# Kernel optimization log

Hardware: AMD Instinct MI355X
Metric: run time of the kernel (lower is better)

Reference implementation:

```python
import jax, jax.numpy as jnp
import numpy as np

DIAG_FLOOR = 0.1
DIAG_CEIL = 1.0


def setup_inputs() -> dict:
    key = jax.random.key(0)
    k1, k2, k3, k4 = jax.random.split(key, 4)
    m, in_f, out_f = 16384, 1024, 2048
    z = jax.random.normal(k1, (m, in_f), dtype=jnp.float32)
    diag_params = jax.random.normal(k2, (out_f, in_f), dtype=jnp.float32)
    mean_params = 5.0 * jax.random.normal(k3, (out_f, in_f, 1), dtype=jnp.float32)
    scale_params = jax.random.normal(k4, (out_f,), dtype=jnp.float32)
    return {"z": z, "diag_params": diag_params, "mean_params": mean_params,
            "scale_params": scale_params}


def reference(z, diag_params, mean_params, scale_params):
    # Clamp diag to (0.1, 1.0) via sigmoid; clamp scale via tanh.
    d = DIAG_FLOOR + (DIAG_CEIL - DIAG_FLOOR) * jax.nn.sigmoid(diag_params)  # (out, in)
    mean = mean_params[..., 0]  # (out, in)

    # Diagonal covariance => quadratic forms reduce to elementwise products:
    # z_cov_z[m,k]    = sum_i d[k,i] * z[m,i]^2
    # mean_cov_mean[k]= sum_i d[k,i] * mean[k,i]^2
    # z_cov_mean[m,k] = sum_i z[m,i] * d[k,i] * mean[k,i]
    z_cov_z = jnp.einsum('mi,ki->mk', z * z, d)          # (m, out)
    mean_cov_mean = jnp.sum(d * mean * mean, axis=1)      # (out,)
    z_cov_mean = jnp.einsum('mi,ki->mk', z, d * mean)     # (m, out)

    scaling = jnp.tanh(scale_params)                      # (out,)
    return scaling * jnp.exp(-z_cov_z - mean_cov_mean + 2.0 * z_cov_mean)
```

## Files before the change

### kernel.cpp

```cpp
#include <hip/hip_runtime.h>
#include <hip/hip_bf16.h>
#include <cstdint>
#include <cstddef>

#define M_DIM 16384
#define IN_F  1024
#define OUT_F 2048
#define K_CAT 2048

typedef float f32x4 __attribute__((ext_vector_type(4)));
typedef short short8 __attribute__((ext_vector_type(8)));

__device__ __forceinline__ void gld_lds16(const void* gptr, void* lptr) {
    __builtin_amdgcn_global_load_lds(
        (const __attribute__((address_space(1))) uint32_t*)gptr,
        (__attribute__((address_space(3))) uint32_t*)lptr,
        16 , 0 , 0 );
}

__global__ __launch_bounds__(256) void prep_z_kernel(const float* __restrict__ z,
                                                     __hip_bfloat16* __restrict__ A) {
    const int idx = blockIdx.x * 256 + threadIdx.x;
    const float4 v = ((const float4*)z)[idx];
    const int m  = idx >> 8;
    const int c4 = (idx & 255) * 4;
    __hip_bfloat16 q[4], r[4];
    q[0] = __float2bfloat16(v.x * v.x); r[0] = __float2bfloat16(v.x);
    q[1] = __float2bfloat16(v.y * v.y); r[1] = __float2bfloat16(v.y);
    q[2] = __float2bfloat16(v.z * v.z); r[2] = __float2bfloat16(v.z);
    q[3] = __float2bfloat16(v.w * v.w); r[3] = __float2bfloat16(v.w);
    __hip_bfloat16* rowp = A + (size_t)m * K_CAT;
    *(uint2*)&rowp[c4]        = *(uint2*)q;
    *(uint2*)&rowp[IN_F + c4] = *(uint2*)r;
}

__global__ __launch_bounds__(256) void prep_b_kernel(const float* __restrict__ diag,
                                                     const float* __restrict__ mean,
                                                     const float* __restrict__ scale,
                                                     __hip_bfloat16* __restrict__ B,
                                                     float* __restrict__ mcm,
                                                     float* __restrict__ ts) {
    const int k = blockIdx.x;
    const int t = threadIdx.x;
    const float4 dp = ((const float4*)(diag + (size_t)k * IN_F))[t];
    const float4 mp = ((const float4*)(mean + (size_t)k * IN_F))[t];
    const float dx[4] = {dp.x, dp.y, dp.z, dp.w};
    const float mx[4] = {mp.x, mp.y, mp.z, mp.w};
    __hip_bfloat16 nb[4], pb[4];
    float acc = 0.f;
#pragma unroll
    for (int j = 0; j < 4; ++j) {
        const float d = 0.1f + 0.9f / (1.f + __expf(-dx[j]));
        nb[j] = __float2bfloat16(-d);
        pb[j] = __float2bfloat16(2.f * d * mx[j]);
        acc += d * mx[j] * mx[j];
    }
    __hip_bfloat16* rowp = B + (size_t)k * K_CAT;
    *(uint2*)&rowp[t * 4]        = *(uint2*)nb;
    *(uint2*)&rowp[IN_F + t * 4] = *(uint2*)pb;
#pragma unroll
    for (int off = 32; off > 0; off >>= 1) acc += __shfl_down(acc, off);
    __shared__ float red[4];
    if ((t & 63) == 0) red[t >> 6] = acc;
    __syncthreads();
    if (t == 0) {
        mcm[k] = red[0] + red[1] + red[2] + red[3];
        ts[k]  = tanhf(scale[k]);
    }
}

__global__ __launch_bounds__(256) void gemm_exp_kernel(
    const __hip_bfloat16* __restrict__ A,
    const __hip_bfloat16* __restrict__ B,
    const float* __restrict__ mcm,
    const float* __restrict__ ts,
    float* __restrict__ out) {
    __shared__ __align__(16) __hip_bfloat16 As[128][64];
    __shared__ __align__(16) __hip_bfloat16 Bs[128][64];

    const int t  = threadIdx.x;
    const int bx = blockIdx.x;
    const int tn = bx & 15;
    const int tm = bx >> 4;

    const int lrow  = t >> 3;
    const int lcol8 = (t & 7) * 8;
    const int wid  = t >> 6;
    const int lane = t & 63;
    const int wm = (wid >> 1) * 64;
    const int wn = (wid & 1) * 64;
    const int l15 = lane & 15;
    const int l4  = lane >> 4;

    f32x4 acc[4][4] = {};

    const __hip_bfloat16* aptr = A + (size_t)(tm * 128 + lrow) * K_CAT + lcol8;
    const __hip_bfloat16* bptr = B + (size_t)(tn * 128 + lrow) * K_CAT + lcol8;

    for (int kt = 0; kt < K_CAT / 64; ++kt) {
#pragma unroll
        for (int j = 0; j < 4; ++j) {
            gld_lds16(aptr + (size_t)j * 32 * K_CAT, &As[j * 32 + lrow][lcol8]);
            gld_lds16(bptr + (size_t)j * 32 * K_CAT, &Bs[j * 32 + lrow][lcol8]);
        }
        aptr += 64;
        bptr += 64;
        __syncthreads();

        short8 af[4][2], bfr[4][2];
#pragma unroll
        for (int fm = 0; fm < 4; ++fm)
#pragma unroll
            for (int kk = 0; kk < 2; ++kk)
                af[fm][kk] = *(const short8*)&As[wm + fm * 16 + l15][kk * 32 + l4 * 8];
#pragma unroll
        for (int fn = 0; fn < 4; ++fn)
#pragma unroll
            for (int kk = 0; kk < 2; ++kk)
                bfr[fn][kk] = *(const short8*)&Bs[wn + fn * 16 + l15][kk * 32 + l4 * 8];
#pragma unroll
        for (int kk = 0; kk < 2; ++kk)
#pragma unroll
            for (int fm = 0; fm < 4; ++fm)
#pragma unroll
                for (int fn = 0; fn < 4; ++fn)
                    acc[fm][fn] = __builtin_amdgcn_mfma_f32_16x16x32_bf16(
                        af[fm][kk], bfr[fn][kk], acc[fm][fn], 0, 0, 0);
        __syncthreads();
    }

#pragma unroll
    for (int fn = 0; fn < 4; ++fn) {
        const int ng = tn * 128 + wn + fn * 16 + l15;
        const float tsv = ts[ng];
        const float mv  = mcm[ng];
#pragma unroll
        for (int fm = 0; fm < 4; ++fm) {
            const int mg0 = tm * 128 + wm + fm * 16 + l4 * 4;
#pragma unroll
            for (int r = 0; r < 4; ++r) {
                out[(size_t)(mg0 + r) * OUT_F + ng] = tsv * __expf(acc[fm][fn][r] - mv);
            }
        }
    }
}

extern "C" void kernel_launch(void* const* d_in, const int* in_sizes, int n_in,
                              void* d_out, int out_size, void* d_ws, size_t ws_size,
                              hipStream_t stream) {
    const float* z     = (const float*)d_in[0];
    const float* diag  = (const float*)d_in[1];
    const float* mean  = (const float*)d_in[2];
    const float* scale = (const float*)d_in[3];
    float* out = (float*)d_out;

    char* ws = (char*)d_ws;
    const size_t A_BYTES = (size_t)M_DIM * K_CAT * sizeof(__hip_bfloat16);
    const size_t B_BYTES = (size_t)OUT_F * K_CAT * sizeof(__hip_bfloat16);
    __hip_bfloat16* Abuf = (__hip_bfloat16*)ws;
    __hip_bfloat16* Bbuf = (__hip_bfloat16*)(ws + A_BYTES);
    float* mcm = (float*)(ws + A_BYTES + B_BYTES);
    float* ts  = (float*)(ws + A_BYTES + B_BYTES + 8192);

    prep_z_kernel<<<(M_DIM * IN_F / 4) / 256, 256, 0, stream>>>(z, Abuf);
    prep_b_kernel<<<OUT_F, 256, 0, stream>>>(diag, mean, scale, Bbuf, mcm, ts);
    gemm_exp_kernel<<<(M_DIM / 128) * (OUT_F / 128), 256, 0, stream>>>(
        Abuf, Bbuf, mcm, ts, out);
}
```

Before: 374.7 us.

## Rewrite GEMM with 256x256 tiles, 4-stage LDS prefetch pipeline and block swizzle

The GEMM moves from 128x128 tiles with 256 threads to 256x256 tiles with 512 threads (8 waves, each doing 128x64). It adds a 4-deep LDS ring buffer fed by direct global-to-LDS loads three K-steps ahead, split into A and B halves interleaved with MFMA phases, using explicit waitcnt, barriers and setprio. A block-index swizzle groups tiles for L2 reuse, and prep_z is widened to 8 elements per thread. The aim is to hide global load latency and raise arithmetic intensity, at the cost of more registers (launch_bounds 512,2), 128KB of LDS per block, and fragile hand scheduling. The 32-wide K steps without padding or swizzle may cause LDS bank conflicts.

```diff
diff --git a/kernel.cpp b/kernel.cpp
--- a/kernel.cpp
+++ b/kernel.cpp
@@ -7,6 +7,7 @@
 #define IN_F  1024
 #define OUT_F 2048
 #define K_CAT 2048
+#define NT    (K_CAT / 32)
 
 typedef float f32x4 __attribute__((ext_vector_type(4)));
 typedef short short8 __attribute__((ext_vector_type(8)));
@@ -21,17 +22,20 @@
 __global__ __launch_bounds__(256) void prep_z_kernel(const float* __restrict__ z,
                                                      __hip_bfloat16* __restrict__ A) {
     const int idx = blockIdx.x * 256 + threadIdx.x;
-    const float4 v = ((const float4*)z)[idx];
-    const int m  = idx >> 8;
-    const int c4 = (idx & 255) * 4;
-    __hip_bfloat16 q[4], r[4];
-    q[0] = __float2bfloat16(v.x * v.x); r[0] = __float2bfloat16(v.x);
-    q[1] = __float2bfloat16(v.y * v.y); r[1] = __float2bfloat16(v.y);
-    q[2] = __float2bfloat16(v.z * v.z); r[2] = __float2bfloat16(v.z);
-    q[3] = __float2bfloat16(v.w * v.w); r[3] = __float2bfloat16(v.w);
+    const int m  = idx >> 7;
+    const int c8 = (idx & 127) * 8;
+    const float4 v0 = ((const float4*)z)[idx * 2];
+    const float4 v1 = ((const float4*)z)[idx * 2 + 1];
+    const float x[8] = {v0.x, v0.y, v0.z, v0.w, v1.x, v1.y, v1.z, v1.w};
+    __hip_bfloat16 q[8], r[8];
+#pragma unroll
+    for (int j = 0; j < 8; ++j) {
+        q[j] = __float2bfloat16(x[j] * x[j]);
+        r[j] = __float2bfloat16(x[j]);
+    }
     __hip_bfloat16* rowp = A + (size_t)m * K_CAT;
-    *(uint2*)&rowp[c4]        = *(uint2*)q;
-    *(uint2*)&rowp[IN_F + c4] = *(uint2*)r;
+    *(uint4*)&rowp[c8]        = *(uint4*)q;
+    *(uint4*)&rowp[IN_F + c8] = *(uint4*)r;
 }
 
 __global__ __launch_bounds__(256) void prep_b_kernel(const float* __restrict__ diag,
@@ -69,78 +73,115 @@
     }
 }
 
-__global__ __launch_bounds__(256) void gemm_exp_kernel(
+__global__ __launch_bounds__(512, 2) void gemm_exp_kernel(
     const __hip_bfloat16* __restrict__ A,
     const __hip_bfloat16* __restrict__ B,
     const float* __restrict__ mcm,
     const float* __restrict__ ts,
     float* __restrict__ out) {
-    __shared__ __align__(16) __hip_bfloat16 As[128][64];
-    __shared__ __align__(16) __hip_bfloat16 Bs[128][64];
-
-    const int t  = threadIdx.x;
-    const int bx = blockIdx.x;
-    const int tn = bx & 15;
-    const int tm = bx >> 4;
-
-    const int lrow  = t >> 3;
-    const int lcol8 = (t & 7) * 8;
-    const int wid  = t >> 6;
-    const int lane = t & 63;
-    const int wm = (wid >> 1) * 64;
-    const int wn = (wid & 1) * 64;
-    const int l15 = lane & 15;
-    const int l4  = lane >> 4;
-
-    f32x4 acc[4][4] = {};
-
-    const __hip_bfloat16* aptr = A + (size_t)(tm * 128 + lrow) * K_CAT + lcol8;
-    const __hip_bfloat16* bptr = B + (size_t)(tn * 128 + lrow) * K_CAT + lcol8;
-
-    for (int kt = 0; kt < K_CAT / 64; ++kt) {
-#pragma unroll
-        for (int j = 0; j < 4; ++j) {
-            gld_lds16(aptr + (size_t)j * 32 * K_CAT, &As[j * 32 + lrow][lcol8]);
-            gld_lds16(bptr + (size_t)j * 32 * K_CAT, &Bs[j * 32 + lrow][lcol8]);
-        }
-        aptr += 64;
-        bptr += 64;
-        __syncthreads();
-
-        short8 af[4][2], bfr[4][2];
+    __shared__ __align__(16) __hip_bfloat16 smem[4][2][8192];
+
+    const int t = threadIdx.x;
+    const int wg = ((blockIdx.x & 7) << 6) | (blockIdx.x >> 3);
+    const int tn = wg & 7;
+    const int tm = wg >> 3;
+
+    const int c0 = t, c1 = t + 512;
+    const int r0 = c0 >> 2, s0 = c0 & 3;
+    const int r1 = c1 >> 2, s1 = c1 & 3;
+    const __hip_bfloat16* gA0 = A + (size_t)(tm * 256 + r0) * K_CAT + s0 * 8;
+    const __hip_bfloat16* gA1 = A + (size_t)(tm * 256 + r1) * K_CAT + s1 * 8;
+    const __hip_bfloat16* gB0 = B + (size_t)(tn * 256 + r0) * K_CAT + s0 * 8;
+    const __hip_bfloat16* gB1 = B + (size_t)(tn * 256 + r1) * K_CAT + s1 * 8;
+
+#define ISSUE_A(buf_, kt_) do { \
+        gld_lds16(gA0 + (kt_) * 32, &smem[buf_][0][c0 * 8]); \
+        gld_lds16(gA1 + (kt_) * 32, &smem[buf_][0][c1 * 8]); } while (0)
+#define ISSUE_B(buf_, kt_) do { \
+        gld_lds16(gB0 + (kt_) * 32, &smem[buf_][1][c0 * 8]); \
+        gld_lds16(gB1 + (kt_) * 32, &smem[buf_][1][c1 * 8]); } while (0)
+
+    const int wid = t >> 6, lane = t & 63;
+    const int wmb = (wid >> 2) * 128;
+    const int wnb = (wid & 3) * 64;
+    const int l15 = lane & 15, l4 = lane >> 4;
+    int offA[8], offB[4];
+#pragma unroll
+    for (int fm = 0; fm < 8; ++fm) offA[fm] = (wmb + fm * 16 + l15) * 32 + l4 * 8;
+#pragma unroll
+    for (int fn = 0; fn < 4; ++fn) offB[fn] = (wnb + fn * 16 + l15) * 32 + l4 * 8;
+
+    f32x4 acc[8][4] = {};
+
+    ISSUE_A(0, 0); ISSUE_B(0, 0);
+    ISSUE_A(1, 1); ISSUE_B(1, 1);
+    ISSUE_A(2, 2); ISSUE_B(2, 2);
+    asm volatile("s_waitcnt vmcnt(8)" ::: "memory");
+    __builtin_amdgcn_s_barrier();
+    __builtin_amdgcn_sched_barrier(0);
+
+#pragma unroll 4
+    for (int kt = 0; kt < NT; ++kt) {
+        const int buf  = kt & 3;
+        const int pf   = (kt < NT - 3) ? kt + 3 : NT - 1;
+        const int pbuf = (kt + 3) & 3;
+
+        short8 bfr[4], af0[4];
+#pragma unroll
+        for (int fn = 0; fn < 4; ++fn) bfr[fn] = *(const short8*)&smem[buf][1][offB[fn]];
+#pragma unroll
+        for (int fm = 0; fm < 4; ++fm) af0[fm] = *(const short8*)&smem[buf][0][offA[fm]];
+        ISSUE_A(pbuf, pf);
+        __builtin_amdgcn_sched_barrier(0);
+        __builtin_amdgcn_s_barrier();
+        asm volatile("s_waitcnt lgkmcnt(0)" ::: "memory");
+        __builtin_amdgcn_sched_barrier(0);
+        __builtin_amdgcn_s_setprio(1);
 #pragma unroll
         for (int fm = 0; fm < 4; ++fm)
 #pragma unroll
-            for (int kk = 0; kk < 2; ++kk)
-                af[fm][kk] = *(const short8*)&As[wm + fm * 16 + l15][kk * 32 + l4 * 8];
-#pragma unroll
-        for (int fn = 0; fn < 4; ++fn)
-#pragma unroll
-            for (int kk = 0; kk < 2; ++kk)
-                bfr[fn][kk] = *(const short8*)&Bs[wn + fn * 16 + l15][kk * 32 + l4 * 8];
-#pragma unroll
-        for (int kk = 0; kk < 2; ++kk)
-#pragma unroll
-            for (int fm = 0; fm < 4; ++fm)
-#pragma unroll
-                for (int fn = 0; fn < 4; ++fn)
-                    acc[fm][fn] = __builtin_amdgcn_mfma_f32_16x16x32_bf16(
-                        af[fm][kk], bfr[fn][kk], acc[fm][fn], 0, 0, 0);
-        __syncthreads();
-    }
+            for (int fn = 0; fn < 4; ++fn)
+                acc[fm][fn] = __builtin_amdgcn_mfma_f32_16x16x32_bf16(
+                    af0[fm], bfr[fn], acc[fm][fn], 0, 0, 0);
+        __builtin_amdgcn_s_setprio(0);
+        __builtin_amdgcn_sched_barrier(0);
+        __builtin_amdgcn_s_barrier();
+
+        short8 af1[4];
+#pragma unroll
+        for (int fm = 0; fm < 4; ++fm) af1[fm] = *(const short8*)&smem[buf][0][offA[fm + 4]];
+        ISSUE_B(pbuf, pf);
+        __builtin_amdgcn_sched_barrier(0);
+        __builtin_amdgcn_s_barrier();
+        asm volatile("s_waitcnt lgkmcnt(0)" ::: "memory");
+        __builtin_amdgcn_sched_barrier(0);
+        __builtin_amdgcn_s_setprio(1);
+#pragma unroll
+        for (int fm = 0; fm < 4; ++fm)
+#pragma unroll
+            for (int fn = 0; fn < 4; ++fn)
+                acc[fm + 4][fn] = __builtin_amdgcn_mfma_f32_16x16x32_bf16(
+                    af1[fm], bfr[fn], acc[fm + 4][fn], 0, 0, 0);
+        __builtin_amdgcn_s_setprio(0);
+        __builtin_amdgcn_sched_barrier(0);
+        asm volatile("s_waitcnt vmcnt(8)" ::: "memory");
+        __builtin_amdgcn_s_barrier();
+        __builtin_amdgcn_sched_barrier(0);
+    }
+#undef ISSUE_A
+#undef ISSUE_B
 
 #pragma unroll
     for (int fn = 0; fn < 4; ++fn) {
-        const int ng = tn * 128 + wn + fn * 16 + l15;
-        const float tsv = ts[ng];
-        const float mv  = mcm[ng];
-#pragma unroll
-        for (int fm = 0; fm < 4; ++fm) {
-            const int mg0 = tm * 128 + wm + fm * 16 + l4 * 4;
-#pragma unroll
-            for (int r = 0; r < 4; ++r) {
-                out[(size_t)(mg0 + r) * OUT_F + ng] = tsv * __expf(acc[fm][fn][r] - mv);
-            }
+        const int gn = tn * 256 + wnb + fn * 16 + l15;
+        const float tsv = ts[gn];
+        const float mv  = mcm[gn];
+#pragma unroll
+        for (int fm = 0; fm < 8; ++fm) {
+            const int gm0 = tm * 256 + wmb + fm * 16 + l4 * 4;
+#pragma unroll
+            for (int r = 0; r < 4; ++r)
+                out[(size_t)(gm0 + r) * OUT_F + gn] = tsv * __expf(acc[fm][fn][r] - mv);
         }
     }
 }
@@ -162,8 +203,8 @@
     float* mcm = (float*)(ws + A_BYTES + B_BYTES);
     float* ts  = (float*)(ws + A_BYTES + B_BYTES + 8192);
 
-    prep_z_kernel<<<(M_DIM * IN_F / 4) / 256, 256, 0, stream>>>(z, Abuf);
+    prep_z_kernel<<<(M_DIM * IN_F / 8) / 256, 256, 0, stream>>>(z, Abuf);
     prep_b_kernel<<<OUT_F, 256, 0, stream>>>(diag, mean, scale, Bbuf, mcm, ts);
-    gemm_exp_kernel<<<(M_DIM / 128) * (OUT_F / 128), 256, 0, stream>>>(
+    gemm_exp_kernel<<<(M_DIM / 256) * (OUT_F / 256), 512, 0, stream>>>(
         Abuf, Bbuf, mcm, ts, out);
 }
```

Result: faster. 324.2 us (-13.5%).
